# Performance work log

Hardware: AMD Instinct MI355X
Metric: run time of the kernel (lower is better)

The kernel has to match this reference:

```python
import jax, jax.numpy as jnp
import numpy as np


def setup_inputs() -> dict:
    key = jax.random.key(0)
    k1, k2 = jax.random.split(key)
    pred_m = jax.random.normal(k1, (64, 1, 512, 512), dtype=jnp.float32)
    # boxes: (x, y, s_x, s_y) per (batch, frame, target); values in [0, 256)
    multi_targets = jax.random.randint(k2, (64, 5, 32, 4), 0, 256, dtype=jnp.int32)
    return {"pred_m": pred_m, "multi_targets": multi_targets}


def _paint_heatmap(multi_targets, B, H, W, dtype):
    """Vectorized replacement for the triple-nested box-fill loop.

    Uses a 2D difference-array scatter + double cumsum: each box adds
    +1/-1 at its four corners; after prefix sums, count>0 marks painted
    pixels (original sets them to 255 regardless of overlap).
    """
    gt = multi_targets.reshape(B, -1, 4)  # [B, N, 4], N = n_frames*n_targets
    x, y, sx, sy = gt[..., 0], gt[..., 1], gt[..., 2], gt[..., 3]
    # python slicing clamps the end of the slice at H/W
    x1 = jnp.minimum(x, H)
    y1 = jnp.minimum(y, W)
    x2 = jnp.minimum(x + sx, H)
    y2 = jnp.minimum(y + sy, W)
    b_idx = jnp.broadcast_to(jnp.arange(B)[:, None], x.shape)
    diff = jnp.zeros((B, H + 1, W + 1), jnp.int32)
    diff = diff.at[b_idx, x1, y1].add(1)
    diff = diff.at[b_idx, x1, y2].add(-1)
    diff = diff.at[b_idx, x2, y1].add(-1)
    diff = diff.at[b_idx, x2, y2].add(1)
    count = jnp.cumsum(jnp.cumsum(diff, axis=1), axis=2)[:, :H, :W]
    return (count > 0).astype(dtype) * jnp.asarray(255.0, dtype)


def reference(pred_m, multi_targets):
    B, _, H, W = pred_m.shape
    heatmap = _paint_heatmap(multi_targets, B, H, W, pred_m.dtype)  # [B, H, W]
    target = heatmap[:, None]            # [B, 1, H, W]
    pred = jax.nn.sigmoid(pred_m)        # [B, 1, H, W]
    smooth = jnp.asarray(1.0, pred_m.dtype)
    intersection = jnp.sum(pred * target, axis=(1, 2, 3))
    pred_sum = jnp.sum(pred, axis=(1, 2, 3))
    target_sum = jnp.sum(target, axis=(1, 2, 3))
    loss = (intersection + smooth) / (pred_sum + target_sum - intersection + smooth)
    return 1.0 - jnp.mean(loss)
```

## Files before the change

### kernel.cpp

```cpp
#include <hip/hip_runtime.h>
#include <math.h>

#define SLICES 16
#define ROWS_PER_SLICE 32
#define NBOXES 160
#define THREADS 256

static __device__ __forceinline__ unsigned umin_(unsigned a, unsigned b) { return a < b ? a : b; }
static __device__ __forceinline__ unsigned umax_(unsigned a, unsigned b) { return a > b ? a : b; }

__global__ __launch_bounds__(THREADS) void paint_reduce_kernel(
    const float* __restrict__ pred, const int* __restrict__ targets,
    double* __restrict__ partials)
{
    __shared__ int s_x1[NBOXES], s_x2[NBOXES];
    __shared__ unsigned s_y1[NBOXES], s_y2[NBOXES];
    __shared__ int s_nbox;
    __shared__ unsigned s_mask[ROWS_PER_SLICE * 16];
    __shared__ double s_red[4 * 3];

    const int t = threadIdx.x;
    const int slice = blockIdx.x;
    const int b = blockIdx.y;
    const int r0 = slice * ROWS_PER_SLICE;

    if (t == 0) s_nbox = 0;
    __syncthreads();

    if (t < NBOXES) {
        const int* g = targets + ((size_t)b * NBOXES + t) * 4;
        int x = g[0], y = g[1], sx = g[2], sy = g[3];
        int x1 = min(x, 512), y1 = min(y, 512);
        int x2 = min(x + sx, 512), y2 = min(y + sy, 512);
        int cx1 = max(x1, r0), cx2 = min(x2, r0 + ROWS_PER_SLICE);
        if (cx2 > cx1 && y2 > y1) {
            int idx = atomicAdd(&s_nbox, 1);
            s_x1[idx] = cx1; s_x2[idx] = cx2;
            s_y1[idx] = (unsigned)y1; s_y2[idx] = (unsigned)y2;
        }
    }
    __syncthreads();

    {
        const int row_l = t >> 3;
        const int w0 = (t & 7) * 2;
        const int r = r0 + row_l;
        unsigned m0 = 0, m1 = 0;
        const unsigned base0 = (unsigned)w0 * 32u;
        const unsigned base1 = base0 + 32u;
        const int nb = s_nbox;
        for (int k = 0; k < nb; ++k) {
            if (r >= s_x1[k] && r < s_x2[k]) {
                unsigned y1 = s_y1[k], y2 = s_y2[k];
                unsigned lo0 = umax_(y1, base0), hi0 = umin_(y2, base0 + 32u);
                if (hi0 > lo0) {
                    unsigned n = hi0 - lo0;
                    unsigned bits = (n == 32u) ? 0xFFFFFFFFu : ((1u << n) - 1u);
                    m0 |= bits << (lo0 - base0);
                }
                unsigned lo1 = umax_(y1, base1), hi1 = umin_(y2, base1 + 32u);
                if (hi1 > lo1) {
                    unsigned n = hi1 - lo1;
                    unsigned bits = (n == 32u) ? 0xFFFFFFFFu : ((1u << n) - 1u);
                    m1 |= bits << (lo1 - base1);
                }
            }
        }
        s_mask[row_l * 16 + w0] = m0;
        s_mask[row_l * 16 + w0 + 1] = m1;
    }
    __syncthreads();

    const float4* p4 = (const float4*)pred;
    const size_t base4 = (size_t)b * 65536 + (size_t)r0 * 128;
    double psum = 0.0, isum = 0.0;
    int cnt = 0;
    for (int i = t; i < ROWS_PER_SLICE * 128; i += THREADS) {
        const int row_l = i >> 7;
        const int col4 = i & 127;
        float4 v = p4[base4 + (size_t)row_l * 128 + col4];
        const unsigned w = s_mask[row_l * 16 + (col4 >> 3)];
        const unsigned bb = (unsigned)(col4 & 7) * 4u;
        float s0 = 1.0f / (1.0f + __expf(-v.x));
        float s1 = 1.0f / (1.0f + __expf(-v.y));
        float s2 = 1.0f / (1.0f + __expf(-v.z));
        float s3 = 1.0f / (1.0f + __expf(-v.w));
        psum += (double)s0 + (double)s1 + (double)s2 + (double)s3;
        if ((w >> bb) & 1u)        { isum += (double)s0; cnt++; }
        if ((w >> (bb + 1)) & 1u)  { isum += (double)s1; cnt++; }
        if ((w >> (bb + 2)) & 1u)  { isum += (double)s2; cnt++; }
        if ((w >> (bb + 3)) & 1u)  { isum += (double)s3; cnt++; }
    }
    double csum = (double)cnt;

    for (int off = 32; off > 0; off >>= 1) {
        psum += __shfl_down(psum, off);
        isum += __shfl_down(isum, off);
        csum += __shfl_down(csum, off);
    }
    const int wave = t >> 6;
    const int lane = t & 63;
    if (lane == 0) {
        s_red[wave * 3 + 0] = psum;
        s_red[wave * 3 + 1] = isum;
        s_red[wave * 3 + 2] = csum;
    }
    __syncthreads();
    if (t == 0) {
        double P = 0, I = 0, C = 0;
        for (int w = 0; w < 4; ++w) {
            P += s_red[w * 3 + 0];
            I += s_red[w * 3 + 1];
            C += s_red[w * 3 + 2];
        }
        double* o = partials + ((size_t)b * SLICES + slice) * 3;
        o[0] = P; o[1] = I; o[2] = C;
    }
}

__global__ __launch_bounds__(64) void final_kernel(
    const double* __restrict__ partials, float* __restrict__ out)
{
    const int b = threadIdx.x;
    double P = 0, I = 0, C = 0;
    for (int s = 0; s < SLICES; ++s) {
        const double* p = partials + ((size_t)b * SLICES + s) * 3;
        P += p[0]; I += p[1]; C += p[2];
    }
    const double inter = 255.0 * I;
    const double tsum  = 255.0 * C;
    double loss = (inter + 1.0) / (P + tsum - inter + 1.0);
    for (int off = 32; off > 0; off >>= 1) loss += __shfl_down(loss, off);
    if (b == 0) out[0] = (float)(1.0 - loss / 64.0);
}

extern "C" void kernel_launch(void* const* d_in, const int* in_sizes, int n_in,
                              void* d_out, int out_size, void* d_ws, size_t ws_size,
                              hipStream_t stream) {
    const float* pred    = (const float*)d_in[0];
    const int*   targets = (const int*)d_in[1];
    float* out = (float*)d_out;
    double* partials = (double*)d_ws;

    dim3 grid(SLICES, 64);
    paint_reduce_kernel<<<grid, THREADS, 0, stream>>>(pred, targets, partials);
    final_kernel<<<1, 64, 0, stream>>>(partials, out);
}
```

Baseline: 114.9 us.

## Use float accumulation, more slices, batched loads and fast sigmoid

Switches per-thread and block accumulation from double to float and uses a hardware reciprocal for the sigmoid, removing costly fp64 adds. The grid now has twice as many blocks of 16 rows each, and the thread-to-word mask mapping is simplified to one word per thread. All float4 loads are issued up front, unrolled, before compute, and the four masked branches become a popcount plus selects. Float partials lose some precision, though the final combine still runs in double.

```diff
diff --git a/kernel.cpp b/kernel.cpp
--- a/kernel.cpp
+++ b/kernel.cpp
@@ -1,23 +1,29 @@
 #include <hip/hip_runtime.h>
 #include <math.h>
 
-#define SLICES 16
-#define ROWS_PER_SLICE 32
+#define SLICES 32
+#define ROWS_PER_SLICE 16
 #define NBOXES 160
 #define THREADS 256
+#define F4_PER_BLOCK (ROWS_PER_SLICE * 128)
+#define F4_PER_THREAD (F4_PER_BLOCK / THREADS)
 
 static __device__ __forceinline__ unsigned umin_(unsigned a, unsigned b) { return a < b ? a : b; }
 static __device__ __forceinline__ unsigned umax_(unsigned a, unsigned b) { return a > b ? a : b; }
 
+static __device__ __forceinline__ float fast_sigmoid(float x) {
+    return __builtin_amdgcn_rcpf(1.0f + __expf(-x));
+}
+
 __global__ __launch_bounds__(THREADS) void paint_reduce_kernel(
     const float* __restrict__ pred, const int* __restrict__ targets,
-    double* __restrict__ partials)
+    float* __restrict__ partials)
 {
     __shared__ int s_x1[NBOXES], s_x2[NBOXES];
     __shared__ unsigned s_y1[NBOXES], s_y2[NBOXES];
     __shared__ int s_nbox;
     __shared__ unsigned s_mask[ROWS_PER_SLICE * 16];
-    __shared__ double s_red[4 * 3];
+    __shared__ float s_red[4 * 3];
 
     const int t = threadIdx.x;
     const int slice = blockIdx.x;
@@ -42,56 +48,57 @@
     __syncthreads();
 
     {
-        const int row_l = t >> 3;
-        const int w0 = (t & 7) * 2;
+        const int row_l = t >> 4;
+        const int w = t & 15;
         const int r = r0 + row_l;
-        unsigned m0 = 0, m1 = 0;
-        const unsigned base0 = (unsigned)w0 * 32u;
-        const unsigned base1 = base0 + 32u;
+        unsigned m = 0;
+        const unsigned base = (unsigned)w * 32u;
         const int nb = s_nbox;
         for (int k = 0; k < nb; ++k) {
             if (r >= s_x1[k] && r < s_x2[k]) {
-                unsigned y1 = s_y1[k], y2 = s_y2[k];
-                unsigned lo0 = umax_(y1, base0), hi0 = umin_(y2, base0 + 32u);
-                if (hi0 > lo0) {
-                    unsigned n = hi0 - lo0;
+                unsigned lo = umax_(s_y1[k], base), hi = umin_(s_y2[k], base + 32u);
+                if (hi > lo) {
+                    unsigned n = hi - lo;
                     unsigned bits = (n == 32u) ? 0xFFFFFFFFu : ((1u << n) - 1u);
-                    m0 |= bits << (lo0 - base0);
-                }
-                unsigned lo1 = umax_(y1, base1), hi1 = umin_(y2, base1 + 32u);
-                if (hi1 > lo1) {
-                    unsigned n = hi1 - lo1;
-                    unsigned bits = (n == 32u) ? 0xFFFFFFFFu : ((1u << n) - 1u);
-                    m1 |= bits << (lo1 - base1);
+                    m |= bits << (lo - base);
                 }
             }
         }
-        s_mask[row_l * 16 + w0] = m0;
-        s_mask[row_l * 16 + w0 + 1] = m1;
+        s_mask[t] = m;
     }
     __syncthreads();
 
     const float4* p4 = (const float4*)pred;
-    const size_t base4 = (size_t)b * 65536 + (size_t)r0 * 128;
-    double psum = 0.0, isum = 0.0;
+    const int col4 = t & 127;
+    const int row_base = t >> 7;
+    const int widx = col4 >> 3;
+    const unsigned bb = (unsigned)(col4 & 7) * 4u;
+    const size_t base4 = (size_t)b * 65536 + (size_t)r0 * 128 + col4;
+
+    float4 v[F4_PER_THREAD];
+    unsigned nib[F4_PER_THREAD];
+#pragma unroll
+    for (int k = 0; k < F4_PER_THREAD; ++k) {
+        const int row = row_base + 2 * k;
+        v[k] = p4[base4 + (size_t)row * 128];
+        nib[k] = (s_mask[row * 16 + widx] >> bb) & 0xFu;
+    }
+
+    float psum = 0.0f, isum = 0.0f;
     int cnt = 0;
-    for (int i = t; i < ROWS_PER_SLICE * 128; i += THREADS) {
-        const int row_l = i >> 7;
-        const int col4 = i & 127;
-        float4 v = p4[base4 + (size_t)row_l * 128 + col4];
-        const unsigned w = s_mask[row_l * 16 + (col4 >> 3)];
-        const unsigned bb = (unsigned)(col4 & 7) * 4u;
-        float s0 = 1.0f / (1.0f + __expf(-v.x));
-        float s1 = 1.0f / (1.0f + __expf(-v.y));
-        float s2 = 1.0f / (1.0f + __expf(-v.z));
-        float s3 = 1.0f / (1.0f + __expf(-v.w));
-        psum += (double)s0 + (double)s1 + (double)s2 + (double)s3;
-        if ((w >> bb) & 1u)        { isum += (double)s0; cnt++; }
-        if ((w >> (bb + 1)) & 1u)  { isum += (double)s1; cnt++; }
-        if ((w >> (bb + 2)) & 1u)  { isum += (double)s2; cnt++; }
-        if ((w >> (bb + 3)) & 1u)  { isum += (double)s3; cnt++; }
+#pragma unroll
+    for (int k = 0; k < F4_PER_THREAD; ++k) {
+        float s0 = fast_sigmoid(v[k].x);
+        float s1 = fast_sigmoid(v[k].y);
+        float s2 = fast_sigmoid(v[k].z);
+        float s3 = fast_sigmoid(v[k].w);
+        psum += (s0 + s1) + (s2 + s3);
+        const unsigned n = nib[k];
+        cnt += __popc(n);
+        isum += ((n & 1u) ? s0 : 0.0f) + ((n & 2u) ? s1 : 0.0f)
+              + ((n & 4u) ? s2 : 0.0f) + ((n & 8u) ? s3 : 0.0f);
     }
-    double csum = (double)cnt;
+    float csum = (float)cnt;
 
     for (int off = 32; off > 0; off >>= 1) {
         psum += __shfl_down(psum, off);
@@ -107,25 +114,25 @@
     }
     __syncthreads();
     if (t == 0) {
-        double P = 0, I = 0, C = 0;
+        float P = 0, I = 0, C = 0;
         for (int w = 0; w < 4; ++w) {
             P += s_red[w * 3 + 0];
             I += s_red[w * 3 + 1];
             C += s_red[w * 3 + 2];
         }
-        double* o = partials + ((size_t)b * SLICES + slice) * 3;
+        float* o = partials + ((size_t)b * SLICES + slice) * 3;
         o[0] = P; o[1] = I; o[2] = C;
     }
 }
 
 __global__ __launch_bounds__(64) void final_kernel(
-    const double* __restrict__ partials, float* __restrict__ out)
+    const float* __restrict__ partials, float* __restrict__ out)
 {
     const int b = threadIdx.x;
     double P = 0, I = 0, C = 0;
     for (int s = 0; s < SLICES; ++s) {
-        const double* p = partials + ((size_t)b * SLICES + s) * 3;
-        P += p[0]; I += p[1]; C += p[2];
+        const float* p = partials + ((size_t)b * SLICES + s) * 3;
+        P += (double)p[0]; I += (double)p[1]; C += (double)p[2];
     }
     const double inter = 255.0 * I;
     const double tsum  = 255.0 * C;
@@ -140,7 +147,7 @@
     const float* pred    = (const float*)d_in[0];
     const int*   targets = (const int*)d_in[1];
     float* out = (float*)d_out;
-    double* partials = (double*)d_ws;
+    float* partials = (float*)d_ws;
 
     dim3 grid(SLICES, 64);
     paint_reduce_kernel<<<grid, THREADS, 0, stream>>>(pred, targets, partials);
```

Measured after the change: 108.3 us. 5.7% less time.
